# Optimization experiments

Hardware: AMD Instinct MI355X
Metric: run time of the kernel (lower is better)

## Reference

```python
import jax, jax.numpy as jnp
import numpy as np

HID = 64      # RNN hidden size (fixed in source)
K = 3         # B-spline order (pykan default)
NUM = 5       # grid intervals (pykan default)
DIMS = [64, 16, 1]  # layer_nums_small_nobi


def make_grid(in_dim):
    # uniform grid on [-1,1] extended by K knots each side -> NUM+2K+1 = 12 knots
    h = 2.0 / NUM
    g = jnp.arange(-K, NUM + K + 1, dtype=jnp.float32) * h - 1.0
    return jnp.broadcast_to(g, (in_dim, g.shape[0]))


def bspline_basis(x, grid):
    # x: (b, in), grid: (in, G) -> basis (b, in, G-K-1) via Cox-de Boor
    xe = x[..., None]
    B = ((xe >= grid[:, :-1]) & (xe < grid[:, 1:])).astype(x.dtype)
    for d in range(1, K + 1):
        left = (xe - grid[:, :-(d + 1)]) / (grid[:, d:-1] - grid[:, :-(d + 1)]) * B[..., :-1]
        right = (grid[:, d + 1:] - xe) / (grid[:, d + 1:] - grid[:, 1:-d]) * B[..., 1:]
        B = left + right
    return B  # (b, in, NUM+K)


def kan_layer(x, grid, coef, sb, sp):
    # coef: (in, out, NUM+K); sb, sp: (in, out)
    bas = bspline_basis(x, grid)                      # (b, in, NUM+K)
    spl = jnp.einsum('bik,iok->bio', bas, coef)       # per-edge spline value
    return jnp.einsum('bi,io->bo', jax.nn.silu(x), sb) + jnp.einsum('bio,io->bo', spl, sp)


def rnn_layer(x, w_ih, w_hh, b_ih, b_hh, return_seq):
    # x: (b, t, f), tanh RNN, h0 = 0
    h0 = jnp.zeros((x.shape[0], HID), x.dtype)
    def step(h, xt):
        h = jnp.tanh(xt @ w_ih.T + h @ w_hh.T + b_ih + b_hh)
        return h, (h if return_seq else 0.0)
    hT, ys = jax.lax.scan(step, h0, jnp.swapaxes(x, 0, 1))
    return jnp.swapaxes(ys, 0, 1) if return_seq else hT


def setup_inputs() -> dict:
    key = jax.random.key(0)
    ks = jax.random.split(key, 16)
    Bsz, T, F = 2048, 256, 64
    s = 1.0 / np.sqrt(HID)
    inp = {'x': jax.random.normal(ks[0], (Bsz, T, F), jnp.float32)}
    inp['w_ih0'] = jax.random.uniform(ks[1], (HID, F), jnp.float32, -s, s)
    inp['w_hh0'] = jax.random.uniform(ks[2], (HID, HID), jnp.float32, -s, s)
    inp['b_ih0'] = jax.random.uniform(ks[3], (HID,), jnp.float32, -s, s)
    inp['b_hh0'] = jax.random.uniform(ks[4], (HID,), jnp.float32, -s, s)
    inp['w_ih1'] = jax.random.uniform(ks[5], (HID, HID), jnp.float32, -s, s)
    inp['w_hh1'] = jax.random.uniform(ks[6], (HID, HID), jnp.float32, -s, s)
    inp['b_ih1'] = jax.random.uniform(ks[7], (HID,), jnp.float32, -s, s)
    inp['b_hh1'] = jax.random.uniform(ks[8], (HID,), jnp.float32, -s, s)
    kk = 9
    for i, (di, do) in enumerate(zip(DIMS[:-1], DIMS[1:])):
        inp[f'grid{i}'] = make_grid(di)
        inp[f'coef{i}'] = 0.1 * jax.random.normal(ks[kk], (di, do, NUM + K), jnp.float32)
        inp[f'sb{i}'] = (1.0 / np.sqrt(di)) * jnp.ones((di, do), jnp.float32) + 0.05 * jax.random.normal(ks[kk + 1], (di, do), jnp.float32)
        inp[f'sp{i}'] = jnp.ones((di, do), jnp.float32)
        kk += 2
    return inp


def reference(x, w_ih0, w_hh0, b_ih0, b_hh0, w_ih1, w_hh1, b_ih1, b_hh1,
              grid0, coef0, sb0, sp0, grid1, coef1, sb1, sp1):
    h1 = rnn_layer(x, w_ih0, w_hh0, b_ih0, b_hh0, return_seq=True)   # (b,t,64)
    out = rnn_layer(h1, w_ih1, w_hh1, b_ih1, b_hh1, return_seq=False)  # last step only
    out = kan_layer(out, grid0, coef0, sb0, sp0)   # (b,16)
    out = kan_layer(out, grid1, coef1, sb1, sp1)   # (b,1)
    return jnp.squeeze(jax.nn.sigmoid(out), 1)     # (b,)
```

## Files before the change

kernel.cpp:

```cpp
#include <hip/hip_runtime.h>
#include <cstdint>
#include <cstddef>

typedef __attribute__((ext_vector_type(8))) __bf16 bf16x8;
typedef __attribute__((ext_vector_type(4))) float f32x4;

#define MFMA16(a, b, c) __builtin_amdgcn_mfma_f32_16x16x32_bf16((a), (b), (c), 0, 0, 0)

__device__ __forceinline__ float fast_tanh(float z) {
    float e = __expf(2.0f * z);
    return 1.0f - 2.0f * __builtin_amdgcn_rcpf(e + 1.0f);
}
__device__ __forceinline__ float fast_sigmoid(float z) {
    return __builtin_amdgcn_rcpf(1.0f + __expf(-z));
}

__device__ __forceinline__ unsigned pk2(float a, float b) {
    union { __bf16 h[2]; unsigned u; } p;
    p.h[0] = (__bf16)a;
    p.h[1] = (__bf16)b;
    return p.u;
}

__device__ __forceinline__ bf16x8 ldwfrag(const float* __restrict__ W, int row, int k0) {
    const float4 a = *(const float4*)(W + row * 64 + k0);
    const float4 b = *(const float4*)(W + row * 64 + k0 + 4);
    bf16x8 f;
    f[0] = (__bf16)a.x; f[1] = (__bf16)a.y; f[2] = (__bf16)a.z; f[3] = (__bf16)a.w;
    f[4] = (__bf16)b.x; f[5] = (__bf16)b.y; f[6] = (__bf16)b.z; f[7] = (__bf16)b.w;
    return f;
}

__device__ __forceinline__ void bspl8(float x, const float* kn, float* B) {
    float b[11];
#pragma unroll
    for (int m = 0; m < 11; ++m)
        b[m] = (x >= kn[m] && x < kn[m + 1]) ? 1.0f : 0.0f;
#pragma unroll
    for (int d = 1; d <= 3; ++d) {
#pragma unroll
        for (int m = 0; m + d < 11; ++m) {
            float lf = (x - kn[m]) / (kn[m + d] - kn[m]) * b[m];
            float rt = (kn[m + d + 1] - x) / (kn[m + d + 1] - kn[m + 1]) * b[m + 1];
            b[m] = lf + rt;
        }
    }
#pragma unroll
    for (int m = 0; m < 8; ++m) B[m] = b[m];
}

__global__ __launch_bounds__(256, 1) void rnn_kan_fused(
    const float* __restrict__ x,
    const float* __restrict__ wih0, const float* __restrict__ whh0,
    const float* __restrict__ bih0, const float* __restrict__ bhh0,
    const float* __restrict__ wih1, const float* __restrict__ whh1,
    const float* __restrict__ bih1, const float* __restrict__ bhh1,
    const float* __restrict__ grid0, const float* __restrict__ coef0,
    const float* __restrict__ sb0, const float* __restrict__ sp0,
    const float* __restrict__ grid1, const float* __restrict__ coef1,
    const float* __restrict__ sb1, const float* __restrict__ sp1,
    float* __restrict__ out)
{
    __shared__ __align__(16) float s_x[4][1024];
    __shared__ __align__(16) unsigned char s_h1[2][2048];
    __shared__ __align__(16) unsigned char s_h2[2][2048];
    __shared__ __align__(16) float s_hf[16][68];
    __shared__ __align__(16) float s_bas[1024][12];
    __shared__ __align__(16) float s_e[16][17];

    const int tid  = threadIdx.x;
    const int wv   = tid >> 6;
    const int lane = tid & 63;
    const int sc   = lane & 15;
    const int gr   = lane >> 4;
    const int s0   = blockIdx.x << 4;

    const int wrow = 16 * wv + sc;
    const int kofs = 8 * gr;
    bf16x8 fWih0[2], fWhh0[2], fWih1[2], fWhh1[2];
#pragma unroll
    for (int kt = 0; kt < 2; ++kt) {
        fWih0[kt] = ldwfrag(wih0, wrow, 32 * kt + kofs);
        fWhh0[kt] = ldwfrag(whh0, wrow, 32 * kt + kofs);
        fWih1[kt] = ldwfrag(wih1, wrow, 32 * kt + kofs);
        fWhh1[kt] = ldwfrag(whh1, wrow, 32 * kt + kofs);
    }
    f32x4 b0v, b1v;
#pragma unroll
    for (int i = 0; i < 4; ++i) {
        const int h = 16 * wv + 4 * gr + i;
        b0v[i] = bih0[h] + bhh0[h];
        b1v[i] = bih1[h] + bhh1[h];
    }

    const int gs = 4 * wv + gr;
    const int gc = (lane & 15) ^ (gs & 7);
    const float* gsrc = x + (size_t)(s0 + gs) * 16384 + gc * 4;
    char* ldsx = (char*)(&s_x[0][0]);

    const unsigned swz  = (unsigned)(sc & 7) << 4;
    const unsigned offW  = sc * 128 + (((unsigned)(32 * wv + 8 * gr)) ^ swz);
    const unsigned offR0 = sc * 128 + (((unsigned)(16 * gr)) ^ swz);
    const unsigned offR1 = sc * 128 + (((unsigned)(64 + 16 * gr)) ^ swz);
    unsigned offX[4];
#pragma unroll
    for (int kt = 0; kt < 2; ++kt)
#pragma unroll
        for (int h = 0; h < 2; ++h)
            offX[2 * kt + h] = sc * 256 + 16 * ((unsigned)(8 * kt + 2 * gr + h) ^ (unsigned)(sc & 7));

#pragma unroll
    for (int t = 0; t < 3; ++t) {
        __builtin_amdgcn_global_load_lds(
            (const __attribute__((address_space(1))) void*)(gsrc + t * 64),
            (__attribute__((address_space(3))) void*)(ldsx + t * 4096 + wv * 1024),
            16, 0, 0);
    }
    asm volatile("s_waitcnt vmcnt(2)" ::: "memory");
    __builtin_amdgcn_s_barrier();
    asm volatile("" ::: "memory");

    bf16x8 h1f[2], h2f[2];
    {
        bf16x8 zf;
#pragma unroll
        for (int e = 0; e < 8; ++e) zf[e] = (__bf16)0.0f;
        h1f[0] = zf; h1f[1] = zf; h2f[0] = zf; h2f[1] = zf;
    }

    f32x4 xw_cur = b0v;
    {
        const char* xb = (const char*)(&s_x[0][0]);
#pragma unroll
        for (int kt = 0; kt < 2; ++kt) {
            const float4 q0 = *(const float4*)(xb + offX[2 * kt + 0]);
            const float4 q1 = *(const float4*)(xb + offX[2 * kt + 1]);
            bf16x8 xa;
            xa[0] = (__bf16)q0.x; xa[1] = (__bf16)q0.y; xa[2] = (__bf16)q0.z; xa[3] = (__bf16)q0.w;
            xa[4] = (__bf16)q1.x; xa[5] = (__bf16)q1.y; xa[6] = (__bf16)q1.z; xa[7] = (__bf16)q1.w;
            xw_cur = MFMA16(fWih0[kt], xa, xw_cur);
        }
    }

    for (int t = 0; t < 256; ++t) {
        const int par = t & 1;
        {
            const int ts = (t + 3 > 255) ? 255 : t + 3;
            __builtin_amdgcn_global_load_lds(
                (const __attribute__((address_space(1))) void*)(gsrc + ts * 64),
                (__attribute__((address_space(3))) void*)(ldsx + ((t + 3) & 3) * 4096 + wv * 1024),
                16, 0, 0);
        }
        f32x4 z1 = xw_cur;
        z1 = MFMA16(fWhh0[0], h1f[0], z1);
        z1 = MFMA16(fWhh0[1], h1f[1], z1);
        f32x4 z2 = b1v;
        z2 = MFMA16(fWih1[0], h1f[0], z2);
        z2 = MFMA16(fWih1[1], h1f[1], z2);
        z2 = MFMA16(fWhh1[0], h2f[0], z2);
        z2 = MFMA16(fWhh1[1], h2f[1], z2);

        float v1[4], v2[4];
#pragma unroll
        for (int i = 0; i < 4; ++i) v1[i] = fast_tanh(z1[i]);
#pragma unroll
        for (int i = 0; i < 4; ++i) v2[i] = fast_tanh(z2[i]);

        uint2 pw1; pw1.x = pk2(v1[0], v1[1]); pw1.y = pk2(v1[2], v1[3]);
        *(uint2*)((char*)(&s_h1[par][0]) + offW) = pw1;
        if (t > 0) {
            uint2 pw2; pw2.x = pk2(v2[0], v2[1]); pw2.y = pk2(v2[2], v2[3]);
            *(uint2*)((char*)(&s_h2[par][0]) + offW) = pw2;
        }

        asm volatile("s_waitcnt vmcnt(2) lgkmcnt(0)" ::: "memory");
        __builtin_amdgcn_s_barrier();
        asm volatile("" ::: "memory");

        h1f[0] = *(const bf16x8*)((const char*)(&s_h1[par][0]) + offR0);
        h1f[1] = *(const bf16x8*)((const char*)(&s_h1[par][0]) + offR1);
        if (t > 0) {
            h2f[0] = *(const bf16x8*)((const char*)(&s_h2[par][0]) + offR0);
            h2f[1] = *(const bf16x8*)((const char*)(&s_h2[par][0]) + offR1);
        }

        {
            const char* xb = (const char*)(&s_x[(t + 1) & 3][0]);
            f32x4 acc = b0v;
#pragma unroll
            for (int kt = 0; kt < 2; ++kt) {
                const float4 q0 = *(const float4*)(xb + offX[2 * kt + 0]);
                const float4 q1 = *(const float4*)(xb + offX[2 * kt + 1]);
                bf16x8 xa;
                xa[0] = (__bf16)q0.x; xa[1] = (__bf16)q0.y; xa[2] = (__bf16)q0.z; xa[3] = (__bf16)q0.w;
                xa[4] = (__bf16)q1.x; xa[5] = (__bf16)q1.y; xa[6] = (__bf16)q1.z; xa[7] = (__bf16)q1.w;
                acc = MFMA16(fWih0[kt], xa, acc);
            }
            xw_cur = acc;
        }
    }

    {
        f32x4 z2 = b1v;
        z2 = MFMA16(fWih1[0], h1f[0], z2);
        z2 = MFMA16(fWih1[1], h1f[1], z2);
        z2 = MFMA16(fWhh1[0], h2f[0], z2);
        z2 = MFMA16(fWhh1[1], h2f[1], z2);
        f32x4 hv;
#pragma unroll
        for (int i = 0; i < 4; ++i) hv[i] = fast_tanh(z2[i]);
        *(f32x4*)(&s_hf[sc][16 * wv + 4 * gr]) = hv;
    }
    __syncthreads();

    float kn0[12], kn1[12];
#pragma unroll
    for (int m = 0; m < 12; ++m) { kn0[m] = grid0[m]; kn1[m] = grid1[m]; }

    for (int q = tid; q < 1024; q += 256) {
        const int i = q >> 4, s = q & 15;
        const float v = s_hf[s][i];
        float B[8];
        bspl8(v, kn0, B);
        *(float4*)(&s_bas[q][0]) = make_float4(B[0], B[1], B[2], B[3]);
        *(float4*)(&s_bas[q][4]) = make_float4(B[4], B[5], B[6], B[7]);
        s_bas[q][8] = v * fast_sigmoid(v);
    }
    __syncthreads();

    {
        const int s = tid >> 4, o = tid & 15;
        float acc = 0.0f;
        for (int i = 0; i < 64; ++i) {
            const int q = (i << 4) + s;
            const float4 B0 = *(const float4*)(&s_bas[q][0]);
            const float4 B1 = *(const float4*)(&s_bas[q][4]);
            const float sil = s_bas[q][8];
            const float* cp = coef0 + i * 128 + o * 8;
            const float4 c0 = *(const float4*)cp;
            const float4 c1 = *(const float4*)(cp + 4);
            const float spl = B0.x * c0.x + B0.y * c0.y + B0.z * c0.z + B0.w * c0.w +
                              B1.x * c1.x + B1.y * c1.y + B1.z * c1.z + B1.w * c1.w;
            acc += sil * sb0[(i << 4) + o] + sp0[(i << 4) + o] * spl;
        }
        float B[8];
        bspl8(acc, kn1, B);
        const float* cp = coef1 + o * 8;
        float spl = 0.0f;
#pragma unroll
        for (int k = 0; k < 8; ++k) spl += B[k] * cp[k];
        s_e[s][o] = (acc * fast_sigmoid(acc)) * sb1[o] + sp1[o] * spl;
    }
    __syncthreads();

    if (tid < 16) {
        float sum = 0.0f;
#pragma unroll
        for (int o = 0; o < 16; ++o) sum += s_e[tid][o];
        out[s0 + tid] = fast_sigmoid(sum);
    }
}

extern "C" void kernel_launch(void* const* d_in, const int* in_sizes, int n_in,
                              void* d_out, int out_size, void* d_ws, size_t ws_size,
                              hipStream_t stream) {
    (void)n_in; (void)out_size; (void)d_ws; (void)ws_size;
    const int B = in_sizes[0] / (256 * 64);
    const int grid = B / 16;
    rnn_kan_fused<<<dim3(grid), dim3(256), 0, stream>>>(
        (const float*)d_in[0],
        (const float*)d_in[1], (const float*)d_in[2], (const float*)d_in[3], (const float*)d_in[4],
        (const float*)d_in[5], (const float*)d_in[6], (const float*)d_in[7], (const float*)d_in[8],
        (const float*)d_in[9], (const float*)d_in[10], (const float*)d_in[11], (const float*)d_in[12],
        (const float*)d_in[13], (const float*)d_in[14], (const float*)d_in[15], (const float*)d_in[16],
        (float*)d_out);
}
```

Baseline: 135.1 us.

## Split MFMA accumulation chains and deepen x prefetch pipeline in RNN recurrence

The serial recurrent MFMA chains are split into independent MFMAs with separate zero or bias accumulators, summed afterwards, so the dependent latency on the per-step critical path is shorter. The h1 tanh and store are issued before the h2 computation. The x prefetch ring grows from 4 to 8 LDS slots with 6 steps of lookahead, and the input projection is computed two steps ahead. This costs extra LDS (16KB more) and registers, plus a few vector adds per step.

```diff
diff --git a/kernel.cpp b/kernel.cpp
--- a/kernel.cpp
+++ b/kernel.cpp
@@ -61,7 +61,7 @@
     const float* __restrict__ sb1, const float* __restrict__ sp1,
     float* __restrict__ out)
 {
-    __shared__ __align__(16) float s_x[4][1024];
+    __shared__ __align__(16) float s_x[8][1024];
     __shared__ __align__(16) unsigned char s_h1[2][2048];
     __shared__ __align__(16) unsigned char s_h2[2][2048];
     __shared__ __align__(16) float s_hf[16][68];
@@ -85,12 +85,13 @@
         fWih1[kt] = ldwfrag(wih1, wrow, 32 * kt + kofs);
         fWhh1[kt] = ldwfrag(whh1, wrow, 32 * kt + kofs);
     }
-    f32x4 b0v, b1v;
+    f32x4 b0v, b1v, zv;
 #pragma unroll
     for (int i = 0; i < 4; ++i) {
         const int h = 16 * wv + 4 * gr + i;
         b0v[i] = bih0[h] + bhh0[h];
         b1v[i] = bih1[h] + bhh1[h];
+        zv[i] = 0.0f;
     }
 
     const int gs = 4 * wv + gr;
@@ -109,28 +110,9 @@
         for (int h = 0; h < 2; ++h)
             offX[2 * kt + h] = sc * 256 + 16 * ((unsigned)(8 * kt + 2 * gr + h) ^ (unsigned)(sc & 7));
 
-#pragma unroll
-    for (int t = 0; t < 3; ++t) {
-        __builtin_amdgcn_global_load_lds(
-            (const __attribute__((address_space(1))) void*)(gsrc + t * 64),
-            (__attribute__((address_space(3))) void*)(ldsx + t * 4096 + wv * 1024),
-            16, 0, 0);
-    }
-    asm volatile("s_waitcnt vmcnt(2)" ::: "memory");
-    __builtin_amdgcn_s_barrier();
-    asm volatile("" ::: "memory");
-
-    bf16x8 h1f[2], h2f[2];
-    {
-        bf16x8 zf;
-#pragma unroll
-        for (int e = 0; e < 8; ++e) zf[e] = (__bf16)0.0f;
-        h1f[0] = zf; h1f[1] = zf; h2f[0] = zf; h2f[1] = zf;
-    }
-
-    f32x4 xw_cur = b0v;
-    {
-        const char* xb = (const char*)(&s_x[0][0]);
+    auto xw_compute = [&](int slot) -> f32x4 {
+        const char* xb = (const char*)(&s_x[slot][0]);
+        f32x4 acc = b0v;
 #pragma unroll
         for (int kt = 0; kt < 2; ++kt) {
             const float4 q0 = *(const float4*)(xb + offX[2 * kt + 0]);
@@ -138,42 +120,66 @@
             bf16x8 xa;
             xa[0] = (__bf16)q0.x; xa[1] = (__bf16)q0.y; xa[2] = (__bf16)q0.z; xa[3] = (__bf16)q0.w;
             xa[4] = (__bf16)q1.x; xa[5] = (__bf16)q1.y; xa[6] = (__bf16)q1.z; xa[7] = (__bf16)q1.w;
-            xw_cur = MFMA16(fWih0[kt], xa, xw_cur);
-        }
-    }
+            acc = MFMA16(fWih0[kt], xa, acc);
+        }
+        return acc;
+    };
+
+#pragma unroll
+    for (int t = 0; t < 6; ++t) {
+        __builtin_amdgcn_global_load_lds(
+            (const __attribute__((address_space(1))) void*)(gsrc + t * 64),
+            (__attribute__((address_space(3))) void*)(ldsx + t * 4096 + wv * 1024),
+            16, 0, 0);
+    }
+    asm volatile("s_waitcnt vmcnt(3)" ::: "memory");
+    __builtin_amdgcn_s_barrier();
+    asm volatile("" ::: "memory");
+
+    bf16x8 h1f[2], h2f[2];
+    {
+        bf16x8 zf;
+#pragma unroll
+        for (int e = 0; e < 8; ++e) zf[e] = (__bf16)0.0f;
+        h1f[0] = zf; h1f[1] = zf; h2f[0] = zf; h2f[1] = zf;
+    }
+
+    f32x4 xw0 = xw_compute(0);
+    f32x4 xw1 = xw_compute(1);
 
     for (int t = 0; t < 256; ++t) {
         const int par = t & 1;
         {
-            const int ts = (t + 3 > 255) ? 255 : t + 3;
+            const int ts = (t + 6 > 255) ? 255 : t + 6;
             __builtin_amdgcn_global_load_lds(
                 (const __attribute__((address_space(1))) void*)(gsrc + ts * 64),
-                (__attribute__((address_space(3))) void*)(ldsx + ((t + 3) & 3) * 4096 + wv * 1024),
+                (__attribute__((address_space(3))) void*)(ldsx + ((t + 6) & 7) * 4096 + wv * 1024),
                 16, 0, 0);
         }
-        f32x4 z1 = xw_cur;
-        z1 = MFMA16(fWhh0[0], h1f[0], z1);
-        z1 = MFMA16(fWhh0[1], h1f[1], z1);
-        f32x4 z2 = b1v;
-        z2 = MFMA16(fWih1[0], h1f[0], z2);
-        z2 = MFMA16(fWih1[1], h1f[1], z2);
-        z2 = MFMA16(fWhh1[0], h2f[0], z2);
-        z2 = MFMA16(fWhh1[1], h2f[1], z2);
-
-        float v1[4], v2[4];
+        f32x4 z1a = MFMA16(fWhh0[0], h1f[0], xw0);
+        f32x4 z1b = MFMA16(fWhh0[1], h1f[1], zv);
+        f32x4 z2a = MFMA16(fWih1[0], h1f[0], b1v);
+        f32x4 z2b = MFMA16(fWih1[1], h1f[1], zv);
+        f32x4 z2c = MFMA16(fWhh1[0], h2f[0], zv);
+        f32x4 z2d = MFMA16(fWhh1[1], h2f[1], zv);
+
+        f32x4 z1 = z1a + z1b;
+        float v1[4];
 #pragma unroll
         for (int i = 0; i < 4; ++i) v1[i] = fast_tanh(z1[i]);
-#pragma unroll
-        for (int i = 0; i < 4; ++i) v2[i] = fast_tanh(z2[i]);
-
         uint2 pw1; pw1.x = pk2(v1[0], v1[1]); pw1.y = pk2(v1[2], v1[3]);
         *(uint2*)((char*)(&s_h1[par][0]) + offW) = pw1;
+
+        f32x4 z2 = (z2a + z2b) + (z2c + z2d);
+        float v2[4];
+#pragma unroll
+        for (int i = 0; i < 4; ++i) v2[i] = fast_tanh(z2[i]);
         if (t > 0) {
             uint2 pw2; pw2.x = pk2(v2[0], v2[1]); pw2.y = pk2(v2[2], v2[3]);
             *(uint2*)((char*)(&s_h2[par][0]) + offW) = pw2;
         }
 
-        asm volatile("s_waitcnt vmcnt(2) lgkmcnt(0)" ::: "memory");
+        asm volatile("s_waitcnt vmcnt(3) lgkmcnt(0)" ::: "memory");
         __builtin_amdgcn_s_barrier();
         asm volatile("" ::: "memory");
 
@@ -184,28 +190,16 @@
             h2f[1] = *(const bf16x8*)((const char*)(&s_h2[par][0]) + offR1);
         }
 
-        {
-            const char* xb = (const char*)(&s_x[(t + 1) & 3][0]);
-            f32x4 acc = b0v;
-#pragma unroll
-            for (int kt = 0; kt < 2; ++kt) {
-                const float4 q0 = *(const float4*)(xb + offX[2 * kt + 0]);
-                const float4 q1 = *(const float4*)(xb + offX[2 * kt + 1]);
-                bf16x8 xa;
-                xa[0] = (__bf16)q0.x; xa[1] = (__bf16)q0.y; xa[2] = (__bf16)q0.z; xa[3] = (__bf16)q0.w;
-                xa[4] = (__bf16)q1.x; xa[5] = (__bf16)q1.y; xa[6] = (__bf16)q1.z; xa[7] = (__bf16)q1.w;
-                acc = MFMA16(fWih0[kt], xa, acc);
-            }
-            xw_cur = acc;
-        }
+        xw0 = xw1;
+        xw1 = xw_compute((t + 2) & 7);
     }
 
     {
-        f32x4 z2 = b1v;
-        z2 = MFMA16(fWih1[0], h1f[0], z2);
-        z2 = MFMA16(fWih1[1], h1f[1], z2);
-        z2 = MFMA16(fWhh1[0], h2f[0], z2);
-        z2 = MFMA16(fWhh1[1], h2f[1], z2);
+        f32x4 z2a = MFMA16(fWih1[0], h1f[0], b1v);
+        f32x4 z2b = MFMA16(fWih1[1], h1f[1], zv);
+        f32x4 z2c = MFMA16(fWhh1[0], h2f[0], zv);
+        f32x4 z2d = MFMA16(fWhh1[1], h2f[1], zv);
+        f32x4 z2 = (z2a + z2b) + (z2c + z2d);
         f32x4 hv;
 #pragma unroll
         for (int i = 0; i < 4; ++i) hv[i] = fast_tanh(z2[i]);
```

Measured after the change: 151.4 us. 1.12x slower.

## Run each sample group in a single wave with cross-lane hidden-state exchange

Applied to the files above, without the earlier changes.

Replaces the 4-wave, 16-sample block with a single-wave block handling 4 samples. All four weight row-tiles are held in registers, and hidden states move between lanes with ds_bpermute instead of LDS writes, reads and a per-step block barrier. The input is loaded directly from global memory into registers, two steps ahead, instead of staged in LDS. The cost is that each wave computes all 16 output columns for 4 samples, so only a quarter of the MFMA output is useful, register pressure rises, and there are four times as many blocks.

```diff
diff --git a/kernel.cpp b/kernel.cpp
--- a/kernel.cpp
+++ b/kernel.cpp
@@ -6,6 +6,7 @@
 typedef __attribute__((ext_vector_type(4))) float f32x4;
 
 #define MFMA16(a, b, c) __builtin_amdgcn_mfma_f32_16x16x32_bf16((a), (b), (c), 0, 0, 0)
+#define BPERM(i, s) __builtin_amdgcn_ds_bpermute((i), (s))
 
 __device__ __forceinline__ float fast_tanh(float z) {
     float e = __expf(2.0f * z);
@@ -15,11 +16,24 @@
     return __builtin_amdgcn_rcpf(1.0f + __expf(-z));
 }
 
-__device__ __forceinline__ unsigned pk2(float a, float b) {
-    union { __bf16 h[2]; unsigned u; } p;
+__device__ __forceinline__ int pk2(float a, float b) {
+    union { __bf16 h[2]; int u; } p;
     p.h[0] = (__bf16)a;
     p.h[1] = (__bf16)b;
     return p.u;
+}
+
+__device__ __forceinline__ bf16x8 frag4(int a, int b, int c, int d) {
+    union { int w[4]; bf16x8 f; } u;
+    u.w[0] = a; u.w[1] = b; u.w[2] = c; u.w[3] = d;
+    return u.f;
+}
+
+__device__ __forceinline__ bf16x8 cvt8(float4 a, float4 b) {
+    bf16x8 f;
+    f[0] = (__bf16)a.x; f[1] = (__bf16)a.y; f[2] = (__bf16)a.z; f[3] = (__bf16)a.w;
+    f[4] = (__bf16)b.x; f[5] = (__bf16)b.y; f[6] = (__bf16)b.z; f[7] = (__bf16)b.w;
+    return f;
 }
 
 __device__ __forceinline__ bf16x8 ldwfrag(const float* __restrict__ W, int row, int k0) {
@@ -31,6 +45,17 @@
     return f;
 }
 
+__device__ __forceinline__ f32x4 sel4(f32x4 a0, f32x4 a1, f32x4 a2, f32x4 a3, int sc) {
+    f32x4 r;
+#pragma unroll
+    for (int i = 0; i < 4; ++i) {
+        float lo = (sc & 4) ? a1[i] : a0[i];
+        float hi = (sc & 4) ? a3[i] : a2[i];
+        r[i] = (sc & 8) ? hi : lo;
+    }
+    return r;
+}
+
 __device__ __forceinline__ void bspl8(float x, const float* kn, float* B) {
     float b[11];
 #pragma unroll
@@ -49,7 +74,7 @@
     for (int m = 0; m < 8; ++m) B[m] = b[m];
 }
 
-__global__ __launch_bounds__(256, 1) void rnn_kan_fused(
+__global__ __launch_bounds__(64, 1) void rnn_kan_wave(
     const float* __restrict__ x,
     const float* __restrict__ wih0, const float* __restrict__ whh0,
     const float* __restrict__ bih0, const float* __restrict__ bhh0,
@@ -61,155 +86,119 @@
     const float* __restrict__ sb1, const float* __restrict__ sp1,
     float* __restrict__ out)
 {
-    __shared__ __align__(16) float s_x[4][1024];
-    __shared__ __align__(16) unsigned char s_h1[2][2048];
-    __shared__ __align__(16) unsigned char s_h2[2][2048];
-    __shared__ __align__(16) float s_hf[16][68];
-    __shared__ __align__(16) float s_bas[1024][12];
-    __shared__ __align__(16) float s_e[16][17];
-
-    const int tid  = threadIdx.x;
-    const int wv   = tid >> 6;
-    const int lane = tid & 63;
-    const int sc   = lane & 15;
-    const int gr   = lane >> 4;
-    const int s0   = blockIdx.x << 4;
-
-    const int wrow = 16 * wv + sc;
-    const int kofs = 8 * gr;
-    bf16x8 fWih0[2], fWhh0[2], fWih1[2], fWhh1[2];
-#pragma unroll
-    for (int kt = 0; kt < 2; ++kt) {
-        fWih0[kt] = ldwfrag(wih0, wrow, 32 * kt + kofs);
-        fWhh0[kt] = ldwfrag(whh0, wrow, 32 * kt + kofs);
-        fWih1[kt] = ldwfrag(wih1, wrow, 32 * kt + kofs);
-        fWhh1[kt] = ldwfrag(whh1, wrow, 32 * kt + kofs);
-    }
-    f32x4 b0v, b1v;
+    __shared__ __align__(16) float s_hf[4][68];
+    __shared__ __align__(16) float s_bas[256][12];
+    __shared__ __align__(16) float s_e[4][17];
+
+    const int lane  = threadIdx.x;
+    const int sc    = lane & 15;
+    const int gr    = lane >> 4;
+    const int samp  = sc & 3;
+    const int rt_own = sc >> 2;
+    const int s0    = blockIdx.x << 2;
+
+    bf16x8 fWih0[4][2], fWhh0[4][2], fWih1[4][2], fWhh1[4][2];
+#pragma unroll
+    for (int rt = 0; rt < 4; ++rt)
+#pragma unroll
+        for (int kt = 0; kt < 2; ++kt) {
+            fWih0[rt][kt] = ldwfrag(wih0, 16 * rt + sc, 32 * kt + 8 * gr);
+            fWhh0[rt][kt] = ldwfrag(whh0, 16 * rt + sc, 32 * kt + 8 * gr);
+            fWih1[rt][kt] = ldwfrag(wih1, 16 * rt + sc, 32 * kt + 8 * gr);
+            fWhh1[rt][kt] = ldwfrag(whh1, 16 * rt + sc, 32 * kt + 8 * gr);
+        }
+
+    f32x4 bo0, bo1, zero;
 #pragma unroll
     for (int i = 0; i < 4; ++i) {
-        const int h = 16 * wv + 4 * gr + i;
-        b0v[i] = bih0[h] + bhh0[h];
-        b1v[i] = bih1[h] + bhh1[h];
-    }
-
-    const int gs = 4 * wv + gr;
-    const int gc = (lane & 15) ^ (gs & 7);
-    const float* gsrc = x + (size_t)(s0 + gs) * 16384 + gc * 4;
-    char* ldsx = (char*)(&s_x[0][0]);
-
-    const unsigned swz  = (unsigned)(sc & 7) << 4;
-    const unsigned offW  = sc * 128 + (((unsigned)(32 * wv + 8 * gr)) ^ swz);
-    const unsigned offR0 = sc * 128 + (((unsigned)(16 * gr)) ^ swz);
-    const unsigned offR1 = sc * 128 + (((unsigned)(64 + 16 * gr)) ^ swz);
-    unsigned offX[4];
-#pragma unroll
-    for (int kt = 0; kt < 2; ++kt)
-#pragma unroll
-        for (int h = 0; h < 2; ++h)
-            offX[2 * kt + h] = sc * 256 + 16 * ((unsigned)(8 * kt + 2 * gr + h) ^ (unsigned)(sc & 7));
-
-#pragma unroll
-    for (int t = 0; t < 3; ++t) {
-        __builtin_amdgcn_global_load_lds(
-            (const __attribute__((address_space(1))) void*)(gsrc + t * 64),
-            (__attribute__((address_space(3))) void*)(ldsx + t * 4096 + wv * 1024),
-            16, 0, 0);
-    }
-    asm volatile("s_waitcnt vmcnt(2)" ::: "memory");
-    __builtin_amdgcn_s_barrier();
-    asm volatile("" ::: "memory");
-
-    bf16x8 h1f[2], h2f[2];
+        const int R = 16 * rt_own + 4 * gr + i;
+        bo0[i] = bih0[R] + bhh0[R];
+        bo1[i] = bih1[R] + bhh1[R];
+        zero[i] = 0.0f;
+    }
+
+    int pidx[8];
+#pragma unroll
+    for (int w = 0; w < 8; ++w) {
+        const int m = 16 * (w >> 2) + 4 * gr + (w & 3);
+        pidx[w] = 4 * (4 * (m >> 3) + samp + 16 * ((m >> 1) & 3));
+    }
+
+    const float* xb = x + (size_t)(s0 + samp) * 16384 + 8 * gr;
+    float4 r0, r1, r2, r3;
+    r0 = *(const float4*)(xb);      r1 = *(const float4*)(xb + 4);
+    r2 = *(const float4*)(xb + 32); r3 = *(const float4*)(xb + 36);
+    bf16x8 xf0 = cvt8(r0, r1), xf1 = cvt8(r2, r3);
+    r0 = *(const float4*)(xb + 64);      r1 = *(const float4*)(xb + 68);
+    r2 = *(const float4*)(xb + 96);      r3 = *(const float4*)(xb + 100);
+
+    bf16x8 h1B0, h1B1, h2B0, h2B1;
     {
         bf16x8 zf;
 #pragma unroll
         for (int e = 0; e < 8; ++e) zf[e] = (__bf16)0.0f;
-        h1f[0] = zf; h1f[1] = zf; h2f[0] = zf; h2f[1] = zf;
-    }
-
-    f32x4 xw_cur = b0v;
+        h1B0 = zf; h1B1 = zf; h2B0 = zf; h2B1 = zf;
+    }
+
+    for (int t = 0; t < 256; ++t) {
+        bf16x8 xn0 = cvt8(r0, r1), xn1 = cvt8(r2, r3);
+        {
+            const float* pn = xb + (size_t)((t + 2 > 255) ? 255 : t + 2) * 64;
+            r0 = *(const float4*)(pn);      r1 = *(const float4*)(pn + 4);
+            r2 = *(const float4*)(pn + 32); r3 = *(const float4*)(pn + 36);
+        }
+
+        f32x4 a[4], c[4];
+#pragma unroll
+        for (int rt = 0; rt < 4; ++rt) {
+            f32x4 t1 = MFMA16(fWih0[rt][0], xf0, zero);
+            t1 = MFMA16(fWih0[rt][1], xf1, t1);
+            t1 = MFMA16(fWhh0[rt][0], h1B0, t1);
+            a[rt] = MFMA16(fWhh0[rt][1], h1B1, t1);
+            f32x4 t2 = MFMA16(fWih1[rt][0], h1B0, zero);
+            t2 = MFMA16(fWih1[rt][1], h1B1, t2);
+            t2 = MFMA16(fWhh1[rt][0], h2B0, t2);
+            c[rt] = MFMA16(fWhh1[rt][1], h2B1, t2);
+        }
+
+        f32x4 oz = sel4(a[0], a[1], a[2], a[3], sc) + bo0;
+        float v[4];
+#pragma unroll
+        for (int i = 0; i < 4; ++i) v[i] = fast_tanh(oz[i]);
+        const int W0 = pk2(v[0], v[1]), W1 = pk2(v[2], v[3]);
+        h1B0 = frag4(BPERM(pidx[0], W0), BPERM(pidx[1], W1),
+                     BPERM(pidx[2], W0), BPERM(pidx[3], W1));
+        h1B1 = frag4(BPERM(pidx[4], W0), BPERM(pidx[5], W1),
+                     BPERM(pidx[6], W0), BPERM(pidx[7], W1));
+
+        f32x4 oz2 = sel4(c[0], c[1], c[2], c[3], sc) + bo1;
+        float u[4];
+#pragma unroll
+        for (int i = 0; i < 4; ++i) u[i] = fast_tanh(oz2[i]);
+        const int U0 = pk2(u[0], u[1]), U1 = pk2(u[2], u[3]);
+        const bf16x8 nh0 = frag4(BPERM(pidx[0], U0), BPERM(pidx[1], U1),
+                                 BPERM(pidx[2], U0), BPERM(pidx[3], U1));
+        const bf16x8 nh1 = frag4(BPERM(pidx[4], U0), BPERM(pidx[5], U1),
+                                 BPERM(pidx[6], U0), BPERM(pidx[7], U1));
+        if (t != 0) { h2B0 = nh0; h2B1 = nh1; }
+
+        xf0 = xn0; xf1 = xn1;
+    }
+
     {
-        const char* xb = (const char*)(&s_x[0][0]);
-#pragma unroll
-        for (int kt = 0; kt < 2; ++kt) {
-            const float4 q0 = *(const float4*)(xb + offX[2 * kt + 0]);
-            const float4 q1 = *(const float4*)(xb + offX[2 * kt + 1]);
-            bf16x8 xa;
-            xa[0] = (__bf16)q0.x; xa[1] = (__bf16)q0.y; xa[2] = (__bf16)q0.z; xa[3] = (__bf16)q0.w;
-            xa[4] = (__bf16)q1.x; xa[5] = (__bf16)q1.y; xa[6] = (__bf16)q1.z; xa[7] = (__bf16)q1.w;
-            xw_cur = MFMA16(fWih0[kt], xa, xw_cur);
-        }
-    }
-
-    for (int t = 0; t < 256; ++t) {
-        const int par = t & 1;
-        {
-            const int ts = (t + 3 > 255) ? 255 : t + 3;
-            __builtin_amdgcn_global_load_lds(
-                (const __attribute__((address_space(1))) void*)(gsrc + ts * 64),
-                (__attribute__((address_space(3))) void*)(ldsx + ((t + 3) & 3) * 4096 + wv * 1024),
-                16, 0, 0);
-        }
-        f32x4 z1 = xw_cur;
-        z1 = MFMA16(fWhh0[0], h1f[0], z1);
-        z1 = MFMA16(fWhh0[1], h1f[1], z1);
-        f32x4 z2 = b1v;
-        z2 = MFMA16(fWih1[0], h1f[0], z2);
-        z2 = MFMA16(fWih1[1], h1f[1], z2);
-        z2 = MFMA16(fWhh1[0], h2f[0], z2);
-        z2 = MFMA16(fWhh1[1], h2f[1], z2);
-
-        float v1[4], v2[4];
-#pragma unroll
-        for (int i = 0; i < 4; ++i) v1[i] = fast_tanh(z1[i]);
-#pragma unroll
-        for (int i = 0; i < 4; ++i) v2[i] = fast_tanh(z2[i]);
-
-        uint2 pw1; pw1.x = pk2(v1[0], v1[1]); pw1.y = pk2(v1[2], v1[3]);
-        *(uint2*)((char*)(&s_h1[par][0]) + offW) = pw1;
-        if (t > 0) {
-            uint2 pw2; pw2.x = pk2(v2[0], v2[1]); pw2.y = pk2(v2[2], v2[3]);
-            *(uint2*)((char*)(&s_h2[par][0]) + offW) = pw2;
-        }
-
-        asm volatile("s_waitcnt vmcnt(2) lgkmcnt(0)" ::: "memory");
-        __builtin_amdgcn_s_barrier();
-        asm volatile("" ::: "memory");
-
-        h1f[0] = *(const bf16x8*)((const char*)(&s_h1[par][0]) + offR0);
-        h1f[1] = *(const bf16x8*)((const char*)(&s_h1[par][0]) + offR1);
-        if (t > 0) {
-            h2f[0] = *(const bf16x8*)((const char*)(&s_h2[par][0]) + offR0);
-            h2f[1] = *(const bf16x8*)((const char*)(&s_h2[par][0]) + offR1);
-        }
-
-        {
-            const char* xb = (const char*)(&s_x[(t + 1) & 3][0]);
-            f32x4 acc = b0v;
-#pragma unroll
-            for (int kt = 0; kt < 2; ++kt) {
-                const float4 q0 = *(const float4*)(xb + offX[2 * kt + 0]);
-                const float4 q1 = *(const float4*)(xb + offX[2 * kt + 1]);
-                bf16x8 xa;
-                xa[0] = (__bf16)q0.x; xa[1] = (__bf16)q0.y; xa[2] = (__bf16)q0.z; xa[3] = (__bf16)q0.w;
-                xa[4] = (__bf16)q1.x; xa[5] = (__bf16)q1.y; xa[6] = (__bf16)q1.z; xa[7] = (__bf16)q1.w;
-                acc = MFMA16(fWih0[kt], xa, acc);
-            }
-            xw_cur = acc;
-        }
-    }
-
-    {
-        f32x4 z2 = b1v;
-        z2 = MFMA16(fWih1[0], h1f[0], z2);
-        z2 = MFMA16(fWih1[1], h1f[1], z2);
-        z2 = MFMA16(fWhh1[0], h2f[0], z2);
-        z2 = MFMA16(fWhh1[1], h2f[1], z2);
+        f32x4 c[4];
+#pragma unroll
+        for (int rt = 0; rt < 4; ++rt) {
+            f32x4 t2 = MFMA16(fWih1[rt][0], h1B0, zero);
+            t2 = MFMA16(fWih1[rt][1], h1B1, t2);
+            t2 = MFMA16(fWhh1[rt][0], h2B0, t2);
+            c[rt] = MFMA16(fWhh1[rt][1], h2B1, t2);
+        }
+        f32x4 oz2 = sel4(c[0], c[1], c[2], c[3], sc) + bo1;
         f32x4 hv;
 #pragma unroll
-        for (int i = 0; i < 4; ++i) hv[i] = fast_tanh(z2[i]);
-        *(f32x4*)(&s_hf[sc][16 * wv + 4 * gr]) = hv;
+        for (int i = 0; i < 4; ++i) hv[i] = fast_tanh(oz2[i]);
+        *(f32x4*)(&s_hf[samp][16 * rt_own + 4 * gr]) = hv;
     }
     __syncthreads();
 
@@ -217,8 +206,10 @@
 #pragma unroll
     for (int m = 0; m < 12; ++m) { kn0[m] = grid0[m]; kn1[m] = grid1[m]; }
 
-    for (int q = tid; q < 1024; q += 256) {
-        const int i = q >> 4, s = q & 15;
+#pragma unroll
+    for (int j = 0; j < 4; ++j) {
+        const int q = lane + 64 * j;
+        const int i = q >> 2, s = q & 3;
         const float v = s_hf[s][i];
         float B[8];
         bspl8(v, kn0, B);
@@ -229,10 +220,10 @@
     __syncthreads();
 
     {
-        const int s = tid >> 4, o = tid & 15;
+        const int s = lane >> 4, o = lane & 15;
         float acc = 0.0f;
         for (int i = 0; i < 64; ++i) {
-            const int q = (i << 4) + s;
+            const int q = (i << 2) + s;
             const float4 B0 = *(const float4*)(&s_bas[q][0]);
             const float4 B1 = *(const float4*)(&s_bas[q][4]);
             const float sil = s_bas[q][8];
@@ -253,11 +244,11 @@
     }
     __syncthreads();
 
-    if (tid < 16) {
+    if (lane < 4) {
         float sum = 0.0f;
 #pragma unroll
-        for (int o = 0; o < 16; ++o) sum += s_e[tid][o];
-        out[s0 + tid] = fast_sigmoid(sum);
+        for (int o = 0; o < 16; ++o) sum += s_e[lane][o];
+        out[s0 + lane] = fast_sigmoid(sum);
     }
 }
 
@@ -266,8 +257,8 @@
                               hipStream_t stream) {
     (void)n_in; (void)out_size; (void)d_ws; (void)ws_size;
     const int B = in_sizes[0] / (256 * 64);
-    const int grid = B / 16;
-    rnn_kan_fused<<<dim3(grid), dim3(256), 0, stream>>>(
+    const int grid = B / 4;
+    rnn_kan_wave<<<dim3(grid), dim3(64), 0, stream>>>(
         (const float*)d_in[0],
         (const float*)d_in[1], (const float*)d_in[2], (const float*)d_in[3], (const float*)d_in[4],
         (const float*)d_in[5], (const float*)d_in[6], (const float*)d_in[7], (const float*)d_in[8],
```

Measured after the change: 247.1 us. +83.0%, slower.
